# Optimization experiments

Measured on AMD Instinct MI355X. Metric: run time of the kernel, lower is better.

## Reference

```python
import jax, jax.numpy as jnp
import numpy as np

B, N, D, E, L = 4, 256, 128, 64, 3  # batch, nodes, node_dim, edge_dim, num_layers
LN_EPS = 1e-5


def setup_inputs() -> dict:
    key = jax.random.key(0)
    ks = jax.random.split(key, 12)

    def w(k, shape, fan_in):
        return jax.random.normal(k, shape, dtype=jnp.float32) / np.float32(np.sqrt(fan_in))

    return {
        "node_features": jax.random.normal(ks[0], (B, N, D), dtype=jnp.float32),
        "adjacency": jax.random.uniform(ks[1], (B, N, N), dtype=jnp.float32),
        # per-layer edge network: Linear(2D->E), ReLU, Linear(E->E)
        "ew1": w(ks[2], (L, 2 * D, E), 2 * D), "eb1": jnp.zeros((L, E), jnp.float32),
        "ew2": w(ks[3], (L, E, E), E),         "eb2": jnp.zeros((L, E), jnp.float32),
        # per-layer message network: Linear(D+E->2D), ReLU, Linear(2D->D)
        "mw1": w(ks[4], (L, D + E, 2 * D), D + E), "mb1": jnp.zeros((L, 2 * D), jnp.float32),
        "mw2": w(ks[5], (L, 2 * D, D), 2 * D),     "mb2": jnp.zeros((L, D), jnp.float32),
        # per-layer update network: Linear(2D->2D), ReLU, Linear(2D->D)
        "uw1": w(ks[6], (L, 2 * D, 2 * D), 2 * D), "ub1": jnp.zeros((L, 2 * D), jnp.float32),
        "uw2": w(ks[7], (L, 2 * D, D), 2 * D),     "ub2": jnp.zeros((L, D), jnp.float32),
        # per-layer LayerNorm
        "ln_g": jnp.ones((L, D), jnp.float32), "ln_b": jnp.zeros((L, D), jnp.float32),
    }


def _layernorm(x, g, b):
    mu = jnp.mean(x, axis=-1, keepdims=True)
    var = jnp.mean(jnp.square(x - mu), axis=-1, keepdims=True)
    return (x - mu) * jax.lax.rsqrt(var + LN_EPS) * g + b


def _forward(node_features, adjacency, ew1, eb1, ew2, eb2, mw1, mb1, mw2, mb2,
             uw1, ub1, uw2, ub2, ln_g, ln_b):
    x = node_features  # [B,N,D]
    for l in range(L):
        # Edge features: edge_input[b,i,j] = cat(x[b,i], x[b,j]); first Linear split to
        # avoid materializing [B,N,N,2D]: cat @ W == x_i @ W_top + x_j @ W_bot.
        w_top, w_bot = ew1[l][:D], ew1[l][D:]
        eh = jax.nn.relu(
            jnp.einsum('bid,de->bie', x, w_top)[:, :, None, :]
            + jnp.einsum('bjd,de->bje', x, w_bot)[:, None, :, :]
            + eb1[l]
        )  # [B,N,N,E]
        edge_feat = jnp.einsum('bije,ef->bijf', eh, ew2[l]) + eb2[l]  # [B,N,N,E]

        # GraphConvLayer: message_input[b,i,j] = cat(x[b,i], edge_feat[b,i,j])
        mw_top, mw_bot = mw1[l][:D], mw1[l][D:]
        mh = jax.nn.relu(
            jnp.einsum('bid,dh->bih', x, mw_top)[:, :, None, :]
            + jnp.einsum('bije,eh->bijh', edge_feat, mw_bot)
            + mb1[l]
        )  # [B,N,N,2D]
        message = jnp.einsum('bijh,hd->bijd', mh, mw2[l]) + mb2[l]  # [B,N,N,D]
        # adjacency-weighted sum over neighbors j (per-node torch loop, vectorized)
        messages = jnp.einsum('bij,bijd->bid', adjacency, message)  # [B,N,D]

        upd_in = jnp.concatenate([x, messages], axis=-1)  # [B,N,2D]
        uh = jax.nn.relu(jnp.einsum('bih,hk->bik', upd_in, uw1[l]) + ub1[l])
        x_new = jnp.einsum('bik,kd->bid', uh, uw2[l]) + ub2[l]  # [B,N,D]

        x = _layernorm(x + x_new, ln_g[l], ln_b[l])
    return x


def reference(node_features, adjacency, ew1, eb1, ew2, eb2, mw1, mb1, mw2, mb2,
              uw1, ub1, uw2, ub2, ln_g, ln_b):
    return _forward(node_features, adjacency, ew1, eb1, ew2, eb2, mw1, mb1, mw2,
                    mb2, uw1, ub1, uw2, ub2, ln_g, ln_b)
```

## Files before the change

### kernel.cpp

```cpp
#include <hip/hip_runtime.h>
#include <hip/hip_bf16.h>


constexpr int cB = 4, cN = 256, cD = 128, cE = 64, cL = 3, cH = 256;
constexpr int RT = 4;
#define LN_EPSF 1e-5f

typedef __attribute__((ext_vector_type(8))) short bf8;
typedef __attribute__((ext_vector_type(4))) float f4;

__device__ __forceinline__ ushort f2bf(float f) {
    uint u = __float_as_uint(f);
    u += 0x7FFFu + ((u >> 16) & 1u);
    return (ushort)(u >> 16);
}

__global__ __launch_bounds__(256) void kW(const float* __restrict__ ew2,
                                          const float* __restrict__ eb2,
                                          const float* __restrict__ mw1,
                                          ushort* __restrict__ W2f,
                                          float* __restrict__ BS2) {
    int bx = blockIdx.x, l = bx >> 3, f0 = (bx & 7) * 8;
    int h = threadIdx.x;
    const float* ew2l = ew2 + l * cE * cE;
    const float* eb2l = eb2 + l * cE;
    const float* mbot = mw1 + l * (cD + cE) * cH + cD * cH;
    float acc[8];
#pragma unroll
    for (int f = 0; f < 8; ++f) acc[f] = 0.f;
    float bacc = 0.f;
    for (int e = 0; e < cE; ++e) {
        float m = mbot[e * cH + h];
        if (f0 == 0) bacc += eb2l[e] * m;
#pragma unroll
        for (int f = 0; f < 8; ++f) acc[f] += ew2l[(f0 + f) * cE + e] * m;
    }
    ushort* W2fl = W2f + l * cE * cH;
    int ht = h >> 4, hc = h & 15;
#pragma unroll
    for (int f = 0; f < 8; ++f) {
        int ff = f0 + f;
        int kc = ff >> 5, lg = (ff >> 3) & 3, e = ff & 7;
        W2fl[((ht * 2 + kc) * 64 + lg * 16 + hc) * 8 + e] = f2bf(acc[f]);
    }
    if (f0 == 0) BS2[l * cH + h] = bacc;
}

__device__ __forceinline__ void proj_1024(const float (*xs)[cD],
                                          float (*ph4)[RT][cH],
                                          float (*pm8)[RT][cD],
                                          int r0, int t,
                                          const float* __restrict__ ew1,
                                          const float* __restrict__ eb1,
                                          const float* __restrict__ mw1,
                                          const float* __restrict__ mb1,
                                          const float* __restrict__ bs2,
                                          float* __restrict__ P1,
                                          float* __restrict__ P2,
                                          float* __restrict__ P3, int nl) {
    {
        int col = t & 255, kc = t >> 8;
        const float* mw1n = mw1 + nl * (cD + cE) * cH;
        float a[RT];
#pragma unroll
        for (int r = 0; r < RT; ++r) a[r] = 0.f;
        for (int k = kc * 32; k < kc * 32 + 32; ++k) {
            float w = mw1n[k * cH + col];
#pragma unroll
            for (int r = 0; r < RT; ++r) a[r] += xs[r][k] * w;
        }
#pragma unroll
        for (int r = 0; r < RT; ++r) ph4[kc][r][col] = a[r];
    }
    {
        int cc = t & 127, kc = t >> 7;
        int which = cc >> 6, e = cc & 63;
        const float* ew1n = ew1 + nl * 2 * cD * cE + which * cD * cE;
        float a[RT];
#pragma unroll
        for (int r = 0; r < RT; ++r) a[r] = 0.f;
        for (int k = kc * 16; k < kc * 16 + 16; ++k) {
            float w = ew1n[k * cE + e];
#pragma unroll
            for (int r = 0; r < RT; ++r) a[r] += xs[r][k] * w;
        }
#pragma unroll
        for (int r = 0; r < RT; ++r) pm8[kc][r][cc] = a[r];
    }
    __syncthreads();
    {
        int r = t >> 8, col = t & 255;
        float v = mb1[nl * cH + col] + bs2[nl * cH + col];
#pragma unroll
        for (int kc = 0; kc < 4; ++kc) v += ph4[kc][r][col];
        P3[(r0 + r) * cH + col] = v;
    }
    if (t < 512) {
        int r = t >> 7, cc = t & 127, which = cc >> 6, e = cc & 63;
        float v = which ? 0.f : eb1[nl * cE + e];
#pragma unroll
        for (int kc = 0; kc < 8; ++kc) v += pm8[kc][r][cc];
        (which ? P2 : P1)[(r0 + r) * cE + e] = v;
    }
}

__global__ __launch_bounds__(1024) void kP(const float* __restrict__ x,
                                           const float* __restrict__ ew1,
                                           const float* __restrict__ eb1,
                                           const float* __restrict__ mw1,
                                           const float* __restrict__ mb1,
                                           const float* __restrict__ bs2,
                                           float* __restrict__ P1,
                                           float* __restrict__ P2,
                                           float* __restrict__ P3) {
    __shared__ float xs[RT][cD];
    __shared__ float ph4[4][RT][cH];
    __shared__ float pm8[8][RT][cD];
    int r0 = blockIdx.x * RT, t = threadIdx.x;
    if (t < 512) {
        int r = t >> 7, d = t & 127;
        xs[r][d] = x[(r0 + r) * cD + d];
    }
    __syncthreads();
    proj_1024(xs, ph4, pm8, r0, t, ew1, eb1, mw1, mb1, bs2, P1, P2, P3, 0);
}

__global__ __launch_bounds__(1024) void kL(const float* __restrict__ x_in,
                                           float* __restrict__ x_out,
                                           const float* __restrict__ P1,
                                           const float* __restrict__ P2,
                                           const float* __restrict__ P3g,
                                           const float* __restrict__ adj,
                                           const ushort* __restrict__ W2f,
                                           const float* __restrict__ mw2,
                                           const float* __restrict__ mb2,
                                           const float* __restrict__ uw1,
                                           const float* __restrict__ ub1,
                                           const float* __restrict__ uw2,
                                           const float* __restrict__ ub2,
                                           const float* __restrict__ lng,
                                           const float* __restrict__ lnb,
                                           float* __restrict__ out,
                                           const float* __restrict__ ew1,
                                           const float* __restrict__ eb1,
                                           const float* __restrict__ mw1,
                                           const float* __restrict__ mb1,
                                           const float* __restrict__ bs2,
                                           float* __restrict__ P1o,
                                           float* __restrict__ P2o,
                                           float* __restrict__ P3o,
                                           int l, int last) {
    __shared__ float sP3[RT][cH];
    __shared__ float sSw[16][cH];
    __shared__ float pm8[8][RT][cD];
    __shared__ float sS[RT][cH];
    __shared__ float uin[RT][cH];
    __shared__ float uh[RT][cH];
    __shared__ float yb[RT][cD];
    __shared__ float xs[RT][cD];
    __shared__ float sAsw[16];
    __shared__ float atots[RT];
    __shared__ float rs1h[RT][2], rs2h[RT][2];

    int bx = blockIdx.x, t = threadIdx.x;
    int r0 = bx * RT;
    int w = t >> 6, ln = t & 63, g = ln >> 4, c = ln & 15;
    int rw = w >> 2, qd = w & 3;
    int bn = r0 + rw;
    int b  = bn >> 8;
    int jw = qd * 64;

    sP3[t >> 8][t & 255] = P3g[(r0 + (t >> 8)) * cH + (t & 255)];

    const float* adjr = adj + bn * cN + jw;
    float adjv[4][4];
    float asum = 0.f;
#pragma unroll
    for (int jt = 0; jt < 4; ++jt)
#pragma unroll
        for (int q = 0; q < 4; ++q) {
            float a = adjr[jt * 16 + g * 4 + q];
            adjv[jt][q] = a;
            asum += a;
        }
    asum += __shfl_xor(asum, 16);
    asum += __shfl_xor(asum, 32);

    const float* p1p = P1 + bn * cE;
    f4 p1lo[2], p1hi[2];
#pragma unroll
    for (int kc = 0; kc < 2; ++kc) {
        p1lo[kc] = *(const f4*)(p1p + kc * 32 + g * 8);
        p1hi[kc] = *(const f4*)(p1p + kc * 32 + g * 8 + 4);
    }

    bf8 af[4][2];
#pragma unroll
    for (int jt = 0; jt < 4; ++jt) {
        const float* p2r = P2 + (b * cN + jw + jt * 16 + c) * cE;
#pragma unroll
        for (int kc = 0; kc < 2; ++kc) {
            f4 v0 = *(const f4*)(p2r + kc * 32 + g * 8);
            f4 v1 = *(const f4*)(p2r + kc * 32 + g * 8 + 4);
            bf8 a;
#pragma unroll
            for (int e = 0; e < 4; ++e) {
                float x0 = v0[e] + p1lo[kc][e]; x0 = x0 > 0.f ? x0 : 0.f;
                float x1 = v1[e] + p1hi[kc][e]; x1 = x1 > 0.f ? x1 : 0.f;
                a[e]     = (short)f2bf(x0);
                a[e + 4] = (short)f2bf(x1);
            }
            af[jt][kc] = a;
        }
    }
    __syncthreads();

    {
        const ushort* W2l = W2f + l * cE * cH;
        bf8 nb0 = *(const bf8*)(W2l + (0 * 64 + ln) * 8);
        bf8 nb1 = *(const bf8*)(W2l + (1 * 64 + ln) * 8);
        for (int ht = 0; ht < 16; ++ht) {
            bf8 b0 = nb0, b1 = nb1;
            if (ht < 15) {
                nb0 = *(const bf8*)(W2l + (((ht + 1) * 2 + 0) * 64 + ln) * 8);
                nb1 = *(const bf8*)(W2l + (((ht + 1) * 2 + 1) * 64 + ln) * 8);
            }
            float p3v = sP3[rw][ht * 16 + c];
            float sp = 0.f;
#pragma unroll
            for (int jt = 0; jt < 4; ++jt) {
                f4 acc = {0.f, 0.f, 0.f, 0.f};
                acc = __builtin_amdgcn_mfma_f32_16x16x32_bf16(af[jt][0], b0, acc, 0, 0, 0);
                acc = __builtin_amdgcn_mfma_f32_16x16x32_bf16(af[jt][1], b1, acc, 0, 0, 0);
#pragma unroll
                for (int q = 0; q < 4; ++q) {
                    float mh = p3v + acc[q];
                    mh = mh > 0.f ? mh : 0.f;
                    sp += adjv[jt][q] * mh;
                }
            }
            sp += __shfl_xor(sp, 16);
            sp += __shfl_xor(sp, 32);
            if (ln < 16) sSw[w][ht * 16 + c] = sp;
        }
    }
    if (ln == 0) sAsw[w] = asum;
    __syncthreads();

    {
        int r = t >> 8, k = t & 255;
        sS[r][k] = sSw[4 * r + 0][k] + sSw[4 * r + 1][k]
                 + sSw[4 * r + 2][k] + sSw[4 * r + 3][k];
    }
    if (t < RT)
        atots[t] = sAsw[4 * t] + sAsw[4 * t + 1] + sAsw[4 * t + 2] + sAsw[4 * t + 3];
    if (t < 512) {
        int r = t >> 7, d = t & 127;
        uin[r][d] = x_in[(r0 + r) * cD + d];
    }
    __syncthreads();

    {
        int cc = t & 127, kc = t >> 7;
        const float* mw2l = mw2 + l * cH * cD;
        float a[RT];
#pragma unroll
        for (int r = 0; r < RT; ++r) a[r] = 0.f;
        for (int k = kc * 32; k < kc * 32 + 32; ++k) {
            float wv = mw2l[k * cD + cc];
#pragma unroll
            for (int r = 0; r < RT; ++r) a[r] += sS[r][k] * wv;
        }
#pragma unroll
        for (int r = 0; r < RT; ++r) pm8[kc][r][cc] = a[r];
    }
    __syncthreads();
    if (t < 512) {
        int r = t >> 7, cc = t & 127;
        float m = atots[r] * mb2[l * cD + cc];
#pragma unroll
        for (int kc = 0; kc < 8; ++kc) m += pm8[kc][r][cc];
        uin[r][cD + cc] = m;
    }
    __syncthreads();

    {
        int col = t & 255, kc = t >> 8;
        const float* uw1l = uw1 + l * cH * cH;
        float a[RT];
#pragma unroll
        for (int r = 0; r < RT; ++r) a[r] = 0.f;
        for (int k = kc * 64; k < kc * 64 + 64; ++k) {
            float wv = uw1l[k * cH + col];
#pragma unroll
            for (int r = 0; r < RT; ++r) a[r] += uin[r][k] * wv;
        }
#pragma unroll
        for (int r = 0; r < RT; ++r) sSw[kc * RT + r][col] = a[r];
    }
    __syncthreads();
    {
        int r = t >> 8, col = t & 255;
        float v = ub1[l * cH + col];
#pragma unroll
        for (int kc = 0; kc < 4; ++kc) v += sSw[kc * RT + r][col];
        uh[r][col] = v > 0.f ? v : 0.f;
    }
    __syncthreads();

    {
        int cc = t & 127, kc = t >> 7;
        const float* uw2l = uw2 + l * cH * cD;
        float a[RT];
#pragma unroll
        for (int r = 0; r < RT; ++r) a[r] = 0.f;
        for (int k = kc * 32; k < kc * 32 + 32; ++k) {
            float wv = uw2l[k * cD + cc];
#pragma unroll
            for (int r = 0; r < RT; ++r) a[r] += uh[r][k] * wv;
        }
#pragma unroll
        for (int r = 0; r < RT; ++r) pm8[kc][r][cc] = a[r];
    }
    __syncthreads();
    if (t < 512) {
        int r = t >> 7, cc = t & 127;
        float v = uin[r][cc] + ub2[l * cD + cc];
#pragma unroll
        for (int kc = 0; kc < 8; ++kc) v += pm8[kc][r][cc];
        yb[r][cc] = v;
    }
    __syncthreads();

    if (t < 512) {
        int r = t >> 7, q = t & 127;
        float y = yb[r][q];
        float s1 = y, s2 = y * y;
#pragma unroll
        for (int o = 1; o < 64; o <<= 1) { s1 += __shfl_xor(s1, o); s2 += __shfl_xor(s2, o); }
        if ((t & 63) == 0) { rs1h[r][q >> 6] = s1; rs2h[r][q >> 6] = s2; }
    }
    __syncthreads();
    if (t < 512) {
        int r = t >> 7, q = t & 127;
        float tot = rs1h[r][0] + rs1h[r][1];
        float tq  = rs2h[r][0] + rs2h[r][1];
        float mu  = tot * (1.f / cD);
        float var = tq * (1.f / cD) - mu * mu;
        float inv = rsqrtf(var + LN_EPSF);
        float res = (yb[r][q] - mu) * inv * lng[l * cD + q] + lnb[l * cD + q];
        x_out[(r0 + r) * cD + q] = res;
        xs[r][q] = res;
        if (last) out[(r0 + r) * cD + q] = res;
    }
    if (last) return;
    __syncthreads();

    proj_1024(xs, reinterpret_cast<float (*)[RT][cH]>(&sSw[0][0]), pm8,
              r0, t, ew1, eb1, mw1, mb1, bs2, P1o, P2o, P3o, l + 1);
}

extern "C" void kernel_launch(void* const* d_in, const int* in_sizes, int n_in,
                              void* d_out, int out_size, void* d_ws, size_t ws_size,
                              hipStream_t stream) {
    (void)in_sizes; (void)n_in; (void)out_size; (void)ws_size;
    const float* nf  = (const float*)d_in[0];
    const float* adj = (const float*)d_in[1];
    const float* ew1 = (const float*)d_in[2];
    const float* eb1 = (const float*)d_in[3];
    const float* ew2 = (const float*)d_in[4];
    const float* eb2 = (const float*)d_in[5];
    const float* mw1 = (const float*)d_in[6];
    const float* mb1 = (const float*)d_in[7];
    const float* mw2 = (const float*)d_in[8];
    const float* mb2 = (const float*)d_in[9];
    const float* uw1 = (const float*)d_in[10];
    const float* ub1 = (const float*)d_in[11];
    const float* uw2 = (const float*)d_in[12];
    const float* ub2 = (const float*)d_in[13];
    const float* lng = (const float*)d_in[14];
    const float* lnb = (const float*)d_in[15];
    float* out = (float*)d_out;

    float* xbuf  = (float*)d_ws;
    float* P1a   = xbuf + cB * cN * cD;
    float* P2a   = P1a  + cB * cN * cE;
    float* P3a   = P2a  + cB * cN * cE;
    float* P1b   = P3a  + cB * cN * cH;
    float* P2b   = P1b  + cB * cN * cE;
    float* P3b   = P2b  + cB * cN * cE;
    float* BS2   = P3b  + cB * cN * cH;
    ushort* W2f  = (ushort*)(BS2 + cL * cH);

    float* P1s[2] = {P1a, P1b};
    float* P2s[2] = {P2a, P2b};
    float* P3s[2] = {P3a, P3b};

    kW<<<cL * 8, 256, 0, stream>>>(ew2, eb2, mw1, W2f, BS2);
    kP<<<cB * cN / RT, 1024, 0, stream>>>(nf, ew1, eb1, mw1, mb1, BS2, P1a, P2a, P3a);
    for (int l = 0; l < cL; ++l) {
        int pi = l & 1, po = (l + 1) & 1;
        kL<<<cB * cN / RT, 1024, 0, stream>>>((l == 0) ? nf : xbuf, xbuf,
                                              P1s[pi], P2s[pi], P3s[pi], adj, W2f,
                                              mw2, mb2, uw1, ub1, uw2, ub2, lng, lnb,
                                              out, ew1, eb1, mw1, mb1, BS2,
                                              P1s[po], P2s[po], P3s[po],
                                              l, l == cL - 1);
    }
}
```

Before: 103.4 us.

## Halve rows per block in layer kernel to 2 with 512-thread blocks

The layer kernel now handles 2 node rows per block with 512 threads instead of 4 rows with 1024 threads, doubling the grid to 512 blocks and asking for 4 blocks per CU through launch bounds. Every dense stage (message MLP second layer, update MLP, LayerNorm, next-layer projection) is re-partitioned across the smaller thread count, and the shared proj_1024 helper is replaced by an inline 2-row projection. This targets better CU fill and latency hiding on a grid that was only 256 blocks. The cost is that each weight matrix is streamed by twice as many blocks, so weight traffic per row goes up.

```diff
diff --git a/kernel.cpp b/kernel.cpp
--- a/kernel.cpp
+++ b/kernel.cpp
@@ -4,6 +4,7 @@
 
 constexpr int cB = 4, cN = 256, cD = 128, cE = 64, cL = 3, cH = 256;
 constexpr int RT = 4;
+constexpr int RL = 2;
 #define LN_EPSF 1e-5f
 
 typedef __attribute__((ext_vector_type(8))) short bf8;
@@ -125,45 +126,45 @@
     proj_1024(xs, ph4, pm8, r0, t, ew1, eb1, mw1, mb1, bs2, P1, P2, P3, 0);
 }
 
-__global__ __launch_bounds__(1024) void kL(const float* __restrict__ x_in,
-                                           float* __restrict__ x_out,
-                                           const float* __restrict__ P1,
-                                           const float* __restrict__ P2,
-                                           const float* __restrict__ P3g,
-                                           const float* __restrict__ adj,
-                                           const ushort* __restrict__ W2f,
-                                           const float* __restrict__ mw2,
-                                           const float* __restrict__ mb2,
-                                           const float* __restrict__ uw1,
-                                           const float* __restrict__ ub1,
-                                           const float* __restrict__ uw2,
-                                           const float* __restrict__ ub2,
-                                           const float* __restrict__ lng,
-                                           const float* __restrict__ lnb,
-                                           float* __restrict__ out,
-                                           const float* __restrict__ ew1,
-                                           const float* __restrict__ eb1,
-                                           const float* __restrict__ mw1,
-                                           const float* __restrict__ mb1,
-                                           const float* __restrict__ bs2,
-                                           float* __restrict__ P1o,
-                                           float* __restrict__ P2o,
-                                           float* __restrict__ P3o,
-                                           int l, int last) {
-    __shared__ float sP3[RT][cH];
-    __shared__ float sSw[16][cH];
-    __shared__ float pm8[8][RT][cD];
-    __shared__ float sS[RT][cH];
-    __shared__ float uin[RT][cH];
-    __shared__ float uh[RT][cH];
-    __shared__ float yb[RT][cD];
-    __shared__ float xs[RT][cD];
-    __shared__ float sAsw[16];
-    __shared__ float atots[RT];
-    __shared__ float rs1h[RT][2], rs2h[RT][2];
+__global__ __launch_bounds__(512, 4) void kL(const float* __restrict__ x_in,
+                                             float* __restrict__ x_out,
+                                             const float* __restrict__ P1,
+                                             const float* __restrict__ P2,
+                                             const float* __restrict__ P3g,
+                                             const float* __restrict__ adj,
+                                             const ushort* __restrict__ W2f,
+                                             const float* __restrict__ mw2,
+                                             const float* __restrict__ mb2,
+                                             const float* __restrict__ uw1,
+                                             const float* __restrict__ ub1,
+                                             const float* __restrict__ uw2,
+                                             const float* __restrict__ ub2,
+                                             const float* __restrict__ lng,
+                                             const float* __restrict__ lnb,
+                                             float* __restrict__ out,
+                                             const float* __restrict__ ew1,
+                                             const float* __restrict__ eb1,
+                                             const float* __restrict__ mw1,
+                                             const float* __restrict__ mb1,
+                                             const float* __restrict__ bs2,
+                                             float* __restrict__ P1o,
+                                             float* __restrict__ P2o,
+                                             float* __restrict__ P3o,
+                                             int l, int last) {
+    __shared__ float sP3[RL][cH];
+    __shared__ float sSw[8][cH];
+    __shared__ float pm[4][RL][cD];
+    __shared__ float sS[RL][cH];
+    __shared__ float uin[RL][cH];
+    __shared__ float uh[RL][cH];
+    __shared__ float yb[RL][cD];
+    __shared__ float xs[RL][cD];
+    __shared__ float sAsw[8];
+    __shared__ float atots[RL];
+    __shared__ float rs1h[RL][2], rs2h[RL][2];
 
     int bx = blockIdx.x, t = threadIdx.x;
-    int r0 = bx * RT;
+    int r0 = bx * RL;
     int w = t >> 6, ln = t & 63, g = ln >> 4, c = ln & 15;
     int rw = w >> 2, qd = w & 3;
     int bn = r0 + rw;
@@ -252,9 +253,9 @@
         sS[r][k] = sSw[4 * r + 0][k] + sSw[4 * r + 1][k]
                  + sSw[4 * r + 2][k] + sSw[4 * r + 3][k];
     }
-    if (t < RT)
+    if (t < RL)
         atots[t] = sAsw[4 * t] + sAsw[4 * t + 1] + sAsw[4 * t + 2] + sAsw[4 * t + 3];
-    if (t < 512) {
+    if (t < RL * cD) {
         int r = t >> 7, d = t & 127;
         uin[r][d] = x_in[(r0 + r) * cD + d];
     }
@@ -263,23 +264,23 @@
     {
         int cc = t & 127, kc = t >> 7;
         const float* mw2l = mw2 + l * cH * cD;
-        float a[RT];
-#pragma unroll
-        for (int r = 0; r < RT; ++r) a[r] = 0.f;
-        for (int k = kc * 32; k < kc * 32 + 32; ++k) {
+        float a[RL];
+#pragma unroll
+        for (int r = 0; r < RL; ++r) a[r] = 0.f;
+        for (int k = kc * 64; k < kc * 64 + 64; ++k) {
             float wv = mw2l[k * cD + cc];
 #pragma unroll
-            for (int r = 0; r < RT; ++r) a[r] += sS[r][k] * wv;
-        }
-#pragma unroll
-        for (int r = 0; r < RT; ++r) pm8[kc][r][cc] = a[r];
-    }
-    __syncthreads();
-    if (t < 512) {
+            for (int r = 0; r < RL; ++r) a[r] += sS[r][k] * wv;
+        }
+#pragma unroll
+        for (int r = 0; r < RL; ++r) pm[kc][r][cc] = a[r];
+    }
+    __syncthreads();
+    if (t < RL * cD) {
         int r = t >> 7, cc = t & 127;
         float m = atots[r] * mb2[l * cD + cc];
 #pragma unroll
-        for (int kc = 0; kc < 8; ++kc) m += pm8[kc][r][cc];
+        for (int kc = 0; kc < 4; ++kc) m += pm[kc][r][cc];
         uin[r][cD + cc] = m;
     }
     __syncthreads();
@@ -287,23 +288,23 @@
     {
         int col = t & 255, kc = t >> 8;
         const float* uw1l = uw1 + l * cH * cH;
-        float a[RT];
-#pragma unroll
-        for (int r = 0; r < RT; ++r) a[r] = 0.f;
-        for (int k = kc * 64; k < kc * 64 + 64; ++k) {
+        float a[RL];
+#pragma unroll
+        for (int r = 0; r < RL; ++r) a[r] = 0.f;
+        for (int k = kc * 128; k < kc * 128 + 128; ++k) {
             float wv = uw1l[k * cH + col];
 #pragma unroll
-            for (int r = 0; r < RT; ++r) a[r] += uin[r][k] * wv;
-        }
-#pragma unroll
-        for (int r = 0; r < RT; ++r) sSw[kc * RT + r][col] = a[r];
+            for (int r = 0; r < RL; ++r) a[r] += uin[r][k] * wv;
+        }
+#pragma unroll
+        for (int r = 0; r < RL; ++r) sSw[kc * RL + r][col] = a[r];
     }
     __syncthreads();
     {
         int r = t >> 8, col = t & 255;
         float v = ub1[l * cH + col];
 #pragma unroll
-        for (int kc = 0; kc < 4; ++kc) v += sSw[kc * RT + r][col];
+        for (int kc = 0; kc < 2; ++kc) v += sSw[kc * RL + r][col];
         uh[r][col] = v > 0.f ? v : 0.f;
     }
     __syncthreads();
@@ -311,28 +312,28 @@
     {
         int cc = t & 127, kc = t >> 7;
         const float* uw2l = uw2 + l * cH * cD;
-        float a[RT];
-#pragma unroll
-        for (int r = 0; r < RT; ++r) a[r] = 0.f;
-        for (int k = kc * 32; k < kc * 32 + 32; ++k) {
+        float a[RL];
+#pragma unroll
+        for (int r = 0; r < RL; ++r) a[r] = 0.f;
+        for (int k = kc * 64; k < kc * 64 + 64; ++k) {
             float wv = uw2l[k * cD + cc];
 #pragma unroll
-            for (int r = 0; r < RT; ++r) a[r] += uh[r][k] * wv;
-        }
-#pragma unroll
-        for (int r = 0; r < RT; ++r) pm8[kc][r][cc] = a[r];
-    }
-    __syncthreads();
-    if (t < 512) {
+            for (int r = 0; r < RL; ++r) a[r] += uh[r][k] * wv;
+        }
+#pragma unroll
+        for (int r = 0; r < RL; ++r) pm[kc][r][cc] = a[r];
+    }
+    __syncthreads();
+    if (t < RL * cD) {
         int r = t >> 7, cc = t & 127;
         float v = uin[r][cc] + ub2[l * cD + cc];
 #pragma unroll
-        for (int kc = 0; kc < 8; ++kc) v += pm8[kc][r][cc];
+        for (int kc = 0; kc < 4; ++kc) v += pm[kc][r][cc];
         yb[r][cc] = v;
     }
     __syncthreads();
 
-    if (t < 512) {
+    if (t < RL * cD) {
         int r = t >> 7, q = t & 127;
         float y = yb[r][q];
         float s1 = y, s2 = y * y;
@@ -341,7 +342,7 @@
         if ((t & 63) == 0) { rs1h[r][q >> 6] = s1; rs2h[r][q >> 6] = s2; }
     }
     __syncthreads();
-    if (t < 512) {
+    if (t < RL * cD) {
         int r = t >> 7, q = t & 127;
         float tot = rs1h[r][0] + rs1h[r][1];
         float tq  = rs2h[r][0] + rs2h[r][1];
@@ -356,8 +357,51 @@
     if (last) return;
     __syncthreads();
 
-    proj_1024(xs, reinterpret_cast<float (*)[RT][cH]>(&sSw[0][0]), pm8,
-              r0, t, ew1, eb1, mw1, mb1, bs2, P1o, P2o, P3o, l + 1);
+    int nl = l + 1;
+    {
+        int col = t & 255, kc = t >> 8;
+        const float* mw1n = mw1 + nl * (cD + cE) * cH;
+        float a[RL];
+#pragma unroll
+        for (int r = 0; r < RL; ++r) a[r] = 0.f;
+        for (int k = kc * 64; k < kc * 64 + 64; ++k) {
+            float wv = mw1n[k * cH + col];
+#pragma unroll
+            for (int r = 0; r < RL; ++r) a[r] += xs[r][k] * wv;
+        }
+#pragma unroll
+        for (int r = 0; r < RL; ++r) sSw[kc * RL + r][col] = a[r];
+    }
+    {
+        int cc = t & 127, kc = t >> 7;
+        int which = cc >> 6, e = cc & 63;
+        const float* ew1n = ew1 + nl * 2 * cD * cE + which * cD * cE;
+        float a[RL];
+#pragma unroll
+        for (int r = 0; r < RL; ++r) a[r] = 0.f;
+        for (int k = kc * 32; k < kc * 32 + 32; ++k) {
+            float wv = ew1n[k * cE + e];
+#pragma unroll
+            for (int r = 0; r < RL; ++r) a[r] += xs[r][k] * wv;
+        }
+#pragma unroll
+        for (int r = 0; r < RL; ++r) pm[kc][r][cc] = a[r];
+    }
+    __syncthreads();
+    {
+        int r = t >> 8, col = t & 255;
+        float v = mb1[nl * cH + col] + bs2[nl * cH + col];
+#pragma unroll
+        for (int kc = 0; kc < 2; ++kc) v += sSw[kc * RL + r][col];
+        P3o[(r0 + r) * cH + col] = v;
+    }
+    if (t < RL * cD) {
+        int r = t >> 7, cc = t & 127, which = cc >> 6, e = cc & 63;
+        float v = which ? 0.f : eb1[nl * cE + e];
+#pragma unroll
+        for (int kc = 0; kc < 4; ++kc) v += pm[kc][r][cc];
+        (which ? P2o : P1o)[(r0 + r) * cE + e] = v;
+    }
 }
 
 extern "C" void kernel_launch(void* const* d_in, const int* in_sizes, int n_in,
@@ -400,11 +444,11 @@
     kP<<<cB * cN / RT, 1024, 0, stream>>>(nf, ew1, eb1, mw1, mb1, BS2, P1a, P2a, P3a);
     for (int l = 0; l < cL; ++l) {
         int pi = l & 1, po = (l + 1) & 1;
-        kL<<<cB * cN / RT, 1024, 0, stream>>>((l == 0) ? nf : xbuf, xbuf,
-                                              P1s[pi], P2s[pi], P3s[pi], adj, W2f,
-                                              mw2, mb2, uw1, ub1, uw2, ub2, lng, lnb,
-                                              out, ew1, eb1, mw1, mb1, BS2,
-                                              P1s[po], P2s[po], P3s[po],
-                                              l, l == cL - 1);
-    }
-}
+        kL<<<cB * cN / RL, 512, 0, stream>>>((l == 0) ? nf : xbuf, xbuf,
+                                             P1s[pi], P2s[pi], P3s[pi], adj, W2f,
+                                             mw2, mb2, uw1, ub1, uw2, ub2, lng, lnb,
+                                             out, ew1, eb1, mw1, mb1, BS2,
+                                             P1s[po], P2s[po], P3s[po],
+                                             l, l == cL - 1);
+    }
+}
```

Result: slower. 150.9 us (+46.0%).

## Pre-transpose dense weights to bf16 and load them as 8-wide vectors

Applied to the files above, without the earlier changes.

Adds a kernel that converts the message, update, and projection weights to bf16 and transposes them so each output column's K-slice is contiguous. The small per-row matmuls then read 16-byte bf8 vectors instead of strided scalar fp32 loads, which halves weight bandwidth and cuts load instruction count. The cost is an extra launch each call plus bf16 rounding of weights that were previously used in full fp32.

```diff
diff --git a/kernel.cpp b/kernel.cpp
--- a/kernel.cpp
+++ b/kernel.cpp
@@ -13,6 +13,9 @@
     uint u = __float_as_uint(f);
     u += 0x7FFFu + ((u >> 16) & 1u);
     return (ushort)(u >> 16);
+}
+__device__ __forceinline__ float bf2f(short v) {
+    return __uint_as_float(((uint)(ushort)v) << 16);
 }
 
 __global__ __launch_bounds__(256) void kW(const float* __restrict__ ew2,
@@ -46,13 +49,39 @@
     if (f0 == 0) BS2[l * cH + h] = bacc;
 }
 
+__global__ __launch_bounds__(256) void kX(const float* __restrict__ mw2,
+                                          const float* __restrict__ uw1,
+                                          const float* __restrict__ uw2,
+                                          const float* __restrict__ mw1,
+                                          const float* __restrict__ ew1,
+                                          ushort* __restrict__ mw2T,
+                                          ushort* __restrict__ uw1T,
+                                          ushort* __restrict__ uw2T,
+                                          ushort* __restrict__ mw1T,
+                                          ushort* __restrict__ ew1T) {
+    int bx = blockIdx.x, l = bx >> 8, k = bx & 255, t = threadIdx.x;
+    uw1T[(l * cH + t) * cH + k] = f2bf(uw1[l * cH * cH + k * cH + t]);
+    if (t < cD) {
+        mw2T[(l * cD + t) * cH + k] = f2bf(mw2[l * cH * cD + k * cD + t]);
+        uw2T[(l * cD + t) * cH + k] = f2bf(uw2[l * cH * cD + k * cD + t]);
+    }
+    if (k < cD) {
+        mw1T[(l * cH + t) * cD + k] = f2bf(mw1[l * (cD + cE) * cH + k * cH + t]);
+        if (t < 128) {
+            int which = t >> 6, e = t & 63;
+            ew1T[(l * 128 + t) * cD + k] =
+                f2bf(ew1[l * 2 * cD * cE + (which * cD + k) * cE + e]);
+        }
+    }
+}
+
 __device__ __forceinline__ void proj_1024(const float (*xs)[cD],
                                           float (*ph4)[RT][cH],
                                           float (*pm8)[RT][cD],
                                           int r0, int t,
-                                          const float* __restrict__ ew1,
+                                          const ushort* __restrict__ ew1T,
                                           const float* __restrict__ eb1,
-                                          const float* __restrict__ mw1,
+                                          const ushort* __restrict__ mw1T,
                                           const float* __restrict__ mb1,
                                           const float* __restrict__ bs2,
                                           float* __restrict__ P1,
@@ -60,29 +89,40 @@
                                           float* __restrict__ P3, int nl) {
     {
         int col = t & 255, kc = t >> 8;
-        const float* mw1n = mw1 + nl * (cD + cE) * cH;
+        const ushort* wp = mw1T + (nl * cH + col) * cD + kc * 32;
         float a[RT];
 #pragma unroll
         for (int r = 0; r < RT; ++r) a[r] = 0.f;
-        for (int k = kc * 32; k < kc * 32 + 32; ++k) {
-            float w = mw1n[k * cH + col];
-#pragma unroll
-            for (int r = 0; r < RT; ++r) a[r] += xs[r][k] * w;
+#pragma unroll
+        for (int kb = 0; kb < 4; ++kb) {
+            bf8 w8 = *(const bf8*)(wp + kb * 8);
+#pragma unroll
+            for (int e = 0; e < 8; ++e) {
+                float wv = bf2f(w8[e]);
+                int k = kc * 32 + kb * 8 + e;
+#pragma unroll
+                for (int r = 0; r < RT; ++r) a[r] += xs[r][k] * wv;
+            }
         }
 #pragma unroll
         for (int r = 0; r < RT; ++r) ph4[kc][r][col] = a[r];
     }
     {
         int cc = t & 127, kc = t >> 7;
-        int which = cc >> 6, e = cc & 63;
-        const float* ew1n = ew1 + nl * 2 * cD * cE + which * cD * cE;
+        const ushort* wp = ew1T + (nl * 128 + cc) * cD + kc * 16;
         float a[RT];
 #pragma unroll
         for (int r = 0; r < RT; ++r) a[r] = 0.f;
-        for (int k = kc * 16; k < kc * 16 + 16; ++k) {
-            float w = ew1n[k * cE + e];
-#pragma unroll
-            for (int r = 0; r < RT; ++r) a[r] += xs[r][k] * w;
+#pragma unroll
+        for (int kb = 0; kb < 2; ++kb) {
+            bf8 w8 = *(const bf8*)(wp + kb * 8);
+#pragma unroll
+            for (int e = 0; e < 8; ++e) {
+                float wv = bf2f(w8[e]);
+                int k = kc * 16 + kb * 8 + e;
+#pragma unroll
+                for (int r = 0; r < RT; ++r) a[r] += xs[r][k] * wv;
+            }
         }
 #pragma unroll
         for (int r = 0; r < RT; ++r) pm8[kc][r][cc] = a[r];
@@ -105,9 +145,9 @@
 }
 
 __global__ __launch_bounds__(1024) void kP(const float* __restrict__ x,
-                                           const float* __restrict__ ew1,
+                                           const ushort* __restrict__ ew1T,
                                            const float* __restrict__ eb1,
-                                           const float* __restrict__ mw1,
+                                           const ushort* __restrict__ mw1T,
                                            const float* __restrict__ mb1,
                                            const float* __restrict__ bs2,
                                            float* __restrict__ P1,
@@ -122,7 +162,7 @@
         xs[r][d] = x[(r0 + r) * cD + d];
     }
     __syncthreads();
-    proj_1024(xs, ph4, pm8, r0, t, ew1, eb1, mw1, mb1, bs2, P1, P2, P3, 0);
+    proj_1024(xs, ph4, pm8, r0, t, ew1T, eb1, mw1T, mb1, bs2, P1, P2, P3, 0);
 }
 
 __global__ __launch_bounds__(1024) void kL(const float* __restrict__ x_in,
@@ -132,18 +172,18 @@
                                            const float* __restrict__ P3g,
                                            const float* __restrict__ adj,
                                            const ushort* __restrict__ W2f,
-                                           const float* __restrict__ mw2,
+                                           const ushort* __restrict__ mw2T,
                                            const float* __restrict__ mb2,
-                                           const float* __restrict__ uw1,
+                                           const ushort* __restrict__ uw1T,
                                            const float* __restrict__ ub1,
-                                           const float* __restrict__ uw2,
+                                           const ushort* __restrict__ uw2T,
                                            const float* __restrict__ ub2,
                                            const float* __restrict__ lng,
                                            const float* __restrict__ lnb,
                                            float* __restrict__ out,
-                                           const float* __restrict__ ew1,
+                                           const ushort* __restrict__ ew1T,
                                            const float* __restrict__ eb1,
-                                           const float* __restrict__ mw1,
+                                           const ushort* __restrict__ mw1T,
                                            const float* __restrict__ mb1,
                                            const float* __restrict__ bs2,
                                            float* __restrict__ P1o,
@@ -262,14 +302,20 @@
 
     {
         int cc = t & 127, kc = t >> 7;
-        const float* mw2l = mw2 + l * cH * cD;
+        const ushort* wp = mw2T + (l * cD + cc) * cH + kc * 32;
         float a[RT];
 #pragma unroll
         for (int r = 0; r < RT; ++r) a[r] = 0.f;
-        for (int k = kc * 32; k < kc * 32 + 32; ++k) {
-            float wv = mw2l[k * cD + cc];
-#pragma unroll
-            for (int r = 0; r < RT; ++r) a[r] += sS[r][k] * wv;
+#pragma unroll
+        for (int kb = 0; kb < 4; ++kb) {
+            bf8 w8 = *(const bf8*)(wp + kb * 8);
+#pragma unroll
+            for (int e = 0; e < 8; ++e) {
+                float wv = bf2f(w8[e]);
+                int k = kc * 32 + kb * 8 + e;
+#pragma unroll
+                for (int r = 0; r < RT; ++r) a[r] += sS[r][k] * wv;
+            }
         }
 #pragma unroll
         for (int r = 0; r < RT; ++r) pm8[kc][r][cc] = a[r];
@@ -286,14 +332,20 @@
 
     {
         int col = t & 255, kc = t >> 8;
-        const float* uw1l = uw1 + l * cH * cH;
+        const ushort* wp = uw1T + (l * cH + col) * cH + kc * 64;
         float a[RT];
 #pragma unroll
         for (int r = 0; r < RT; ++r) a[r] = 0.f;
-        for (int k = kc * 64; k < kc * 64 + 64; ++k) {
-            float wv = uw1l[k * cH + col];
-#pragma unroll
-            for (int r = 0; r < RT; ++r) a[r] += uin[r][k] * wv;
+#pragma unroll
+        for (int kb = 0; kb < 8; ++kb) {
+            bf8 w8 = *(const bf8*)(wp + kb * 8);
+#pragma unroll
+            for (int e = 0; e < 8; ++e) {
+                float wv = bf2f(w8[e]);
+                int k = kc * 64 + kb * 8 + e;
+#pragma unroll
+                for (int r = 0; r < RT; ++r) a[r] += uin[r][k] * wv;
+            }
         }
 #pragma unroll
         for (int r = 0; r < RT; ++r) sSw[kc * RT + r][col] = a[r];
@@ -310,14 +362,20 @@
 
     {
         int cc = t & 127, kc = t >> 7;
-        const float* uw2l = uw2 + l * cH * cD;
+        const ushort* wp = uw2T + (l * cD + cc) * cH + kc * 32;
         float a[RT];
 #pragma unroll
         for (int r = 0; r < RT; ++r) a[r] = 0.f;
-        for (int k = kc * 32; k < kc * 32 + 32; ++k) {
-            float wv = uw2l[k * cD + cc];
-#pragma unroll
-            for (int r = 0; r < RT; ++r) a[r] += uh[r][k] * wv;
+#pragma unroll
+        for (int kb = 0; kb < 4; ++kb) {
+            bf8 w8 = *(const bf8*)(wp + kb * 8);
+#pragma unroll
+            for (int e = 0; e < 8; ++e) {
+                float wv = bf2f(w8[e]);
+                int k = kc * 32 + kb * 8 + e;
+#pragma unroll
+                for (int r = 0; r < RT; ++r) a[r] += uh[r][k] * wv;
+            }
         }
 #pragma unroll
         for (int r = 0; r < RT; ++r) pm8[kc][r][cc] = a[r];
@@ -357,7 +415,7 @@
     __syncthreads();
 
     proj_1024(xs, reinterpret_cast<float (*)[RT][cH]>(&sSw[0][0]), pm8,
-              r0, t, ew1, eb1, mw1, mb1, bs2, P1o, P2o, P3o, l + 1);
+              r0, t, ew1T, eb1, mw1T, mb1, bs2, P1o, P2o, P3o, l + 1);
 }
 
 extern "C" void kernel_launch(void* const* d_in, const int* in_sizes, int n_in,
@@ -391,20 +449,28 @@
     float* P3b   = P2b  + cB * cN * cE;
     float* BS2   = P3b  + cB * cN * cH;
     ushort* W2f  = (ushort*)(BS2 + cL * cH);
+    ushort* mw2T = W2f  + cL * cE * cH;
+    ushort* uw1T = mw2T + cL * cD * cH;
+    ushort* uw2T = uw1T + cL * cH * cH;
+    ushort* mw1T = uw2T + cL * cD * cH;
+    ushort* ew1T = mw1T + cL * cH * cD;
 
     float* P1s[2] = {P1a, P1b};
     float* P2s[2] = {P2a, P2b};
     float* P3s[2] = {P3a, P3b};
 
     kW<<<cL * 8, 256, 0, stream>>>(ew2, eb2, mw1, W2f, BS2);
-    kP<<<cB * cN / RT, 1024, 0, stream>>>(nf, ew1, eb1, mw1, mb1, BS2, P1a, P2a, P3a);
+    kX<<<cL * 256, 256, 0, stream>>>(mw2, uw1, uw2, mw1, ew1,
+                                     mw2T, uw1T, uw2T, mw1T, ew1T);
+    kP<<<cB * cN / RT, 1024, 0, stream>>>(nf, ew1T, eb1, mw1T, mb1, BS2,
+                                          P1a, P2a, P3a);
     for (int l = 0; l < cL; ++l) {
         int pi = l & 1, po = (l + 1) & 1;
         kL<<<cB * cN / RT, 1024, 0, stream>>>((l == 0) ? nf : xbuf, xbuf,
                                               P1s[pi], P2s[pi], P3s[pi], adj, W2f,
-                                              mw2, mb2, uw1, ub1, uw2, ub2, lng, lnb,
-                                              out, ew1, eb1, mw1, mb1, BS2,
-                                              P1s[po], P2s[po], P3s[po],
+                                              mw2T, mb2, uw1T, ub1, uw2T, ub2,
+                                              lng, lnb, out, ew1T, eb1, mw1T, mb1,
+                                              BS2, P1s[po], P2s[po], P3s[po],
                                               l, l == cL - 1);
     }
 }
```

Result: slower. 125.1 us (+21.0%).
